# Kernel tuning notes

Measured on AMD Instinct MI355X. Metric: run time of the kernel, lower is better.

Reference implementation:

```python
import jax, jax.numpy as jnp
import numpy as np

HIDDEN_SIZE = 1024  # used for scaling, per the module's __init__
NEG_INF = -1e9

def setup_inputs() -> dict:
    key = jax.random.key(0)
    kq, kk, kv, km = jax.random.split(key, 4)
    B, H, S, D = 2, 16, 2048, 64
    query = jax.random.normal(kq, (B, H, S, D), dtype=jnp.float32)
    k_ = jax.random.normal(kk, (B, H, S, D), dtype=jnp.float32)
    v_ = jax.random.normal(kv, (B, H, S, D), dtype=jnp.float32)
    mask = jax.random.randint(km, (B, S), 0, 2, dtype=jnp.int32)
    return {"query": query, "key": k_, "value": v_, "mask": mask}

def reference(query, key, value, mask):
    # scores: [B,H,S,S]
    scores = jnp.einsum("bhqd,bhkd->bhqk", query, key)
    scores = scores / jnp.sqrt(jnp.float32(HIDDEN_SIZE))
    m = mask.astype(jnp.float32)[:, None, None, :]  # [B,1,1,S]
    scores = scores + NEG_INF * (1.0 - m)
    weights = jax.nn.softmax(scores, axis=-1)
    return jnp.einsum("bhqk,bhkd->bhqd", weights, value)
```

## Files before the change

kernel.cpp:

```cpp
#include <hip/hip_runtime.h>
#include <hip/hip_bf16.h>

typedef __bf16 bf16x8 __attribute__((ext_vector_type(8)));
typedef __bf16 bf16x4 __attribute__((ext_vector_type(4)));
typedef float  f32x4  __attribute__((ext_vector_type(4)));

constexpr int SEQ = 2048;
constexpr int HD  = 64;
constexpr int KT  = 64;
constexpr int QB  = 64;
constexpr int NT  = SEQ / KT;
constexpr int LDP = 72;

__global__ __launch_bounds__(256)
void prepass(const float* __restrict__ K, const float* __restrict__ V,
             __bf16* __restrict__ Kf, __bf16* __restrict__ Vf)
{
    const int t = blockIdx.x, bh = blockIdx.y, tid = threadIdx.x;
    const size_t base = (size_t)bh * SEQ * HD;
    __bf16* kd = Kf + (size_t)(bh * NT + t) * 4096;
    __bf16* vd = Vf + (size_t)(bh * NT + t) * 4096;

    #pragma unroll
    for (int p = 0; p < 2; ++p) {
        int gran = p * 256 + tid;
        int frag = gran >> 6, l = gran & 63, lo = l & 15, hi = l >> 4;
        int s = frag >> 1, kh = frag & 1;
        const float* src = K + base + (size_t)(t*64 + s*16 + lo) * HD + kh*32 + hi*8;
        float4 a = *(const float4*)src, c = *(const float4*)(src + 4);
        bf16x8 o;
        o[0]=(__bf16)a.x; o[1]=(__bf16)a.y; o[2]=(__bf16)a.z; o[3]=(__bf16)a.w;
        o[4]=(__bf16)c.x; o[5]=(__bf16)c.y; o[6]=(__bf16)c.z; o[7]=(__bf16)c.w;
        *(bf16x8*)(kd + gran * 8) = o;
    }
    #pragma unroll
    for (int p = 0; p < 2; ++p) {
        int gran = p * 256 + tid;
        int frag = gran >> 6, l = gran & 63, lo = l & 15, hi = l >> 4;
        int nt = frag >> 1, kh = frag & 1;
        const float* src = V + base + (size_t)(t*64 + kh*32 + hi*8) * HD + nt*16 + lo;
        bf16x8 o;
        #pragma unroll
        for (int j = 0; j < 8; ++j) o[j] = (__bf16)src[j * HD];
        *(bf16x8*)(vd + gran * 8) = o;
    }
}

__global__ __launch_bounds__(256, 4)
void attn_fwd3(const float* __restrict__ Q, const __bf16* __restrict__ Kf,
               const __bf16* __restrict__ Vf, const int* __restrict__ mask,
               float* __restrict__ out)
{
    __shared__ __bf16 Pl[4][16][LDP];
    __shared__ unsigned long long Ml[NT];

    const int tid = threadIdx.x;
    const int w   = tid >> 6;
    const int l   = tid & 63;
    const int lo  = l & 15;
    const int hi  = l >> 4;

    const int id   = blockIdx.x;
    const int virt = (id & 7) * 128 + (id >> 3);
    const int bh   = virt >> 5;
    const int qb   = virt & 31;
    const int b    = bh >> 4;
    const size_t base = (size_t)bh * SEQ * HD;
    const int qbase = qb * QB + w * 16;

    {
        const int4* mp = (const int4*)(mask + b * SEQ);
        int4 m0 = mp[tid * 2], m1 = mp[tid * 2 + 1];
        unsigned byte =
            ((unsigned)(m0.x != 0)     ) | ((unsigned)(m0.y != 0) << 1) |
            ((unsigned)(m0.z != 0) << 2) | ((unsigned)(m0.w != 0) << 3) |
            ((unsigned)(m1.x != 0) << 4) | ((unsigned)(m1.y != 0) << 5) |
            ((unsigned)(m1.z != 0) << 6) | ((unsigned)(m1.w != 0) << 7);
        ((unsigned char*)Ml)[tid] = (unsigned char)byte;
    }

    bf16x8 qf[2];
    {
        const float* qp = Q + base + (size_t)(qbase + lo) * HD;
        #pragma unroll
        for (int kh = 0; kh < 2; ++kh) {
            const float4 a = *(const float4*)(qp + kh*32 + hi*8);
            const float4 c = *(const float4*)(qp + kh*32 + hi*8 + 4);
            bf16x8 f;
            f[0]=(__bf16)a.x; f[1]=(__bf16)a.y; f[2]=(__bf16)a.z; f[3]=(__bf16)a.w;
            f[4]=(__bf16)c.x; f[5]=(__bf16)c.y; f[6]=(__bf16)c.z; f[7]=(__bf16)c.w;
            qf[kh] = f;
        }
    }

    __syncthreads();

    f32x4 acc[4] = {{0,0,0,0},{0,0,0,0},{0,0,0,0},{0,0,0,0}};
    float m_run = -INFINITY, l_run = 0.f;

    const __bf16* Kb = Kf + (size_t)bh * NT * 4096 + l * 8;
    const __bf16* Vb = Vf + (size_t)bh * NT * 4096 + l * 8;

    for (int t = 0; t < NT; ++t) {
        const __bf16* Kt = Kb + (size_t)t * 4096;
        const __bf16* Vt = Vb + (size_t)t * 4096;

        float sv[4][4];
        const unsigned long long mb = Ml[t];
        #pragma unroll
        for (int s = 0; s < 4; ++s) {
            bf16x8 k0 = *(const bf16x8*)(Kt + (s*2+0) * 512);
            bf16x8 k1 = *(const bf16x8*)(Kt + (s*2+1) * 512);
            f32x4 c = {0,0,0,0};
            c = __builtin_amdgcn_mfma_f32_16x16x32_bf16(k0, qf[0], c, 0, 0, 0);
            c = __builtin_amdgcn_mfma_f32_16x16x32_bf16(k1, qf[1], c, 0, 0, 0);
            const unsigned ms = (unsigned)(mb >> (s * 16));
            #pragma unroll
            for (int r = 0; r < 4; ++r)
                sv[s][r] = c[r] * 0.03125f +
                           (((ms >> (hi*4 + r)) & 1u) ? 0.f : -1e9f);
        }

        bf16x8 vfr[8];
        #pragma unroll
        for (int f = 0; f < 8; ++f) vfr[f] = *(const bf16x8*)(Vt + f * 512);

        float tmx[4], tsm[4];
        #pragma unroll
        for (int s = 0; s < 4; ++s)
            tmx[s] = fmaxf(fmaxf(sv[s][0], sv[s][1]), fmaxf(sv[s][2], sv[s][3]));
        float pm = fmaxf(fmaxf(tmx[0], tmx[1]), fmaxf(tmx[2], tmx[3]));
        pm = fmaxf(pm, __shfl_xor(pm, 16));
        pm = fmaxf(pm, __shfl_xor(pm, 32));

        const float mn  = fmaxf(m_run, pm);
        const float scl = __expf(m_run - mn);
        m_run = mn;

        float p[4][4];
        #pragma unroll
        for (int s = 0; s < 4; ++s) {
            #pragma unroll
            for (int r = 0; r < 4; ++r)
                p[s][r] = __expf(sv[s][r] - mn);
            tsm[s] = (p[s][0] + p[s][1]) + (p[s][2] + p[s][3]);
        }
        float rs = (tsm[0] + tsm[1]) + (tsm[2] + tsm[3]);
        rs += __shfl_xor(rs, 16);
        rs += __shfl_xor(rs, 32);
        l_run = l_run * scl + rs;

        #pragma unroll
        for (int nt = 0; nt < 4; ++nt)
            #pragma unroll
            for (int r = 0; r < 4; ++r)
                acc[nt][r] *= scl;

        #pragma unroll
        for (int s = 0; s < 4; ++s)
            #pragma unroll
            for (int r = 0; r < 4; ++r)
                Pl[w][lo][s*16 + hi*4 + r] = (__bf16)p[s][r];

        bf16x8 pa0 = *(const bf16x8*)&Pl[w][lo][hi * 8];
        bf16x8 pa1 = *(const bf16x8*)&Pl[w][lo][32 + hi * 8];
        #pragma unroll
        for (int nt = 0; nt < 4; ++nt) {
            acc[nt] = __builtin_amdgcn_mfma_f32_16x16x32_bf16(vfr[nt*2+0], pa0, acc[nt], 0, 0, 0);
            acc[nt] = __builtin_amdgcn_mfma_f32_16x16x32_bf16(vfr[nt*2+1], pa1, acc[nt], 0, 0, 0);
        }
    }

    const float inv = 1.0f / l_run;
    float* op = out + base + (size_t)(qbase + lo) * HD;
    #pragma unroll
    for (int nt = 0; nt < 4; ++nt)
        #pragma unroll
        for (int r = 0; r < 4; ++r)
            op[nt*16 + hi*4 + r] = acc[nt][r] * inv;
}

__global__ __launch_bounds__(256)
void attn_fwd_legacy(const float* __restrict__ Q, const float* __restrict__ K,
                     const float* __restrict__ V, const int* __restrict__ mask,
                     float* __restrict__ out)
{
    __shared__ __bf16 Kl[KT][LDP];
    __shared__ __bf16 Vl[HD][LDP];
    __shared__ __bf16 Pl[4][16][LDP];

    const int tid = threadIdx.x;
    const int w   = tid >> 6;
    const int l   = tid & 63;
    const int lo  = l & 15;
    const int hi  = l >> 4;

    const int bh = blockIdx.y;
    const int b  = bh >> 4;
    const size_t base = (size_t)bh * SEQ * HD;
    const int qbase = blockIdx.x * QB + w * 16;

    bf16x8 qf[2];
    {
        const float* qp = Q + base + (size_t)(qbase + lo) * HD;
        #pragma unroll
        for (int kh = 0; kh < 2; ++kh) {
            const float4 a = *(const float4*)(qp + kh*32 + hi*8);
            const float4 c = *(const float4*)(qp + kh*32 + hi*8 + 4);
            bf16x8 f;
            f[0]=(__bf16)a.x; f[1]=(__bf16)a.y; f[2]=(__bf16)a.z; f[3]=(__bf16)a.w;
            f[4]=(__bf16)c.x; f[5]=(__bf16)c.y; f[6]=(__bf16)c.z; f[7]=(__bf16)c.w;
            qf[kh] = f;
        }
    }

    f32x4 acc[4] = {{0,0,0,0},{0,0,0,0},{0,0,0,0},{0,0,0,0}};
    float m_run[4], l_run[4];
    #pragma unroll
    for (int r = 0; r < 4; ++r) { m_run[r] = -INFINITY; l_run[r] = 0.f; }

    const int* maskp = mask + b * SEQ;

    for (int k0 = 0; k0 < SEQ; k0 += KT) {
        #pragma unroll
        for (int i = 0; i < 4; ++i) {
            int e4 = i * 256 + tid;
            int key = e4 >> 4, d4 = (e4 & 15) * 4;
            float4 kv = *(const float4*)(K + base + (size_t)(k0 + key) * HD + d4);
            bf16x4 kb;
            kb[0]=(__bf16)kv.x; kb[1]=(__bf16)kv.y; kb[2]=(__bf16)kv.z; kb[3]=(__bf16)kv.w;
            *(bf16x4*)&Kl[key][d4] = kb;
        }
        #pragma unroll
        for (int i = 0; i < 4; ++i) {
            int e4 = i * 256 + tid;
            int key = e4 >> 4, d4 = (e4 & 15) * 4;
            float4 vv = *(const float4*)(V + base + (size_t)(k0 + key) * HD + d4);
            Vl[d4+0][key] = (__bf16)vv.x;
            Vl[d4+1][key] = (__bf16)vv.y;
            Vl[d4+2][key] = (__bf16)vv.z;
            Vl[d4+3][key] = (__bf16)vv.w;
        }
        __syncthreads();

        float sv[4][4];
        #pragma unroll
        for (int s = 0; s < 4; ++s) {
            f32x4 c = {0,0,0,0};
            bf16x8 kf0 = *(const bf16x8*)&Kl[s*16 + lo][hi*8];
            bf16x8 kf1 = *(const bf16x8*)&Kl[s*16 + lo][32 + hi*8];
            c = __builtin_amdgcn_mfma_f32_16x16x32_bf16(qf[0], kf0, c, 0, 0, 0);
            c = __builtin_amdgcn_mfma_f32_16x16x32_bf16(qf[1], kf1, c, 0, 0, 0);
            const int km = maskp[k0 + s*16 + lo];
            #pragma unroll
            for (int r = 0; r < 4; ++r)
                sv[s][r] = km ? (c[r] * 0.03125f) : -1e9f;
        }

        float tm[4];
        #pragma unroll
        for (int r = 0; r < 4; ++r)
            tm[r] = fmaxf(fmaxf(sv[0][r], sv[1][r]), fmaxf(sv[2][r], sv[3][r]));
        #pragma unroll
        for (int off = 1; off < 16; off <<= 1)
            #pragma unroll
            for (int r = 0; r < 4; ++r)
                tm[r] = fmaxf(tm[r], __shfl_xor(tm[r], off));

        float scl[4];
        #pragma unroll
        for (int r = 0; r < 4; ++r) {
            float mn = fmaxf(m_run[r], tm[r]);
            scl[r] = __expf(m_run[r] - mn);
            m_run[r] = mn;
        }
        float pv_[4][4], rs[4] = {0.f, 0.f, 0.f, 0.f};
        #pragma unroll
        for (int s = 0; s < 4; ++s)
            #pragma unroll
            for (int r = 0; r < 4; ++r) {
                float p = __expf(sv[s][r] - m_run[r]);
                pv_[s][r] = p;
                rs[r] += p;
            }
        #pragma unroll
        for (int off = 1; off < 16; off <<= 1)
            #pragma unroll
            for (int r = 0; r < 4; ++r)
                rs[r] += __shfl_xor(rs[r], off);
        #pragma unroll
        for (int r = 0; r < 4; ++r)
            l_run[r] = l_run[r] * scl[r] + rs[r];
        #pragma unroll
        for (int nt = 0; nt < 4; ++nt)
            #pragma unroll
            for (int r = 0; r < 4; ++r)
                acc[nt][r] *= scl[r];

        #pragma unroll
        for (int s = 0; s < 4; ++s)
            #pragma unroll
            for (int r = 0; r < 4; ++r)
                Pl[w][hi*4 + r][s*16 + lo] = (__bf16)pv_[s][r];

        bf16x8 pa0 = *(const bf16x8*)&Pl[w][lo][hi*8];
        bf16x8 pa1 = *(const bf16x8*)&Pl[w][lo][32 + hi*8];
        #pragma unroll
        for (int nt = 0; nt < 4; ++nt) {
            bf16x8 v0 = *(const bf16x8*)&Vl[nt*16 + lo][hi*8];
            bf16x8 v1 = *(const bf16x8*)&Vl[nt*16 + lo][32 + hi*8];
            acc[nt] = __builtin_amdgcn_mfma_f32_16x16x32_bf16(pa0, v0, acc[nt], 0, 0, 0);
            acc[nt] = __builtin_amdgcn_mfma_f32_16x16x32_bf16(pa1, v1, acc[nt], 0, 0, 0);
        }
        __syncthreads();
    }

    float inv[4];
    #pragma unroll
    for (int r = 0; r < 4; ++r) inv[r] = 1.0f / l_run[r];
    float* op = out + base + (size_t)qbase * HD;
    #pragma unroll
    for (int nt = 0; nt < 4; ++nt)
        #pragma unroll
        for (int r = 0; r < 4; ++r)
            op[(size_t)(hi*4 + r) * HD + nt*16 + lo] = acc[nt][r] * inv[r];
}

extern "C" void kernel_launch(void* const* d_in, const int* in_sizes, int n_in,
                              void* d_out, int out_size, void* d_ws, size_t ws_size,
                              hipStream_t stream) {
    (void)in_sizes; (void)n_in; (void)out_size;
    const float* Q  = (const float*)d_in[0];
    const float* K  = (const float*)d_in[1];
    const float* V  = (const float*)d_in[2];
    const int* mask = (const int*)d_in[3];
    float* out      = (float*)d_out;

    const size_t kv_elems = (size_t)32 * SEQ * HD;
    const size_t need = kv_elems * 2  * 2 ;

    if (ws_size >= need) {
        __bf16* Kf = (__bf16*)d_ws;
        __bf16* Vf = Kf + kv_elems;
        hipLaunchKernelGGL(prepass, dim3(NT, 32), dim3(256), 0, stream, K, V, Kf, Vf);
        hipLaunchKernelGGL(attn_fwd3, dim3(1024), dim3(256), 0, stream,
                           Q, Kf, Vf, mask, out);
    } else {
        hipLaunchKernelGGL(attn_fwd_legacy, dim3(SEQ / QB, 32), dim3(256), 0, stream,
                           Q, K, V, mask, out);
    }
}
```

Baseline: 168.7 us.

## Add lazy softmax rescaling, deferred row-sum reduction, setprio, and LDS-staged prepass

The online-softmax loop now skips the cross-lane max reduction and accumulator rescale unless some lane's tile max exceeds the running max by more than 8. The per-tile row-sum shuffles are replaced by per-lane partial sums that are reduced once at the end. The P matrix is written to LDS as packed bf16x4 stores, and s_setprio brackets the MFMA sections. The K/V prepass stages tiles through shared memory so the V transpose reads coalesced global data, at the cost of an extra LDS round trip and barrier.

After: 161.2 us. -4.5%, faster.

```diff
diff --git a/kernel.cpp b/kernel.cpp
--- a/kernel.cpp
+++ b/kernel.cpp
@@ -16,33 +16,41 @@
 void prepass(const float* __restrict__ K, const float* __restrict__ V,
              __bf16* __restrict__ Kf, __bf16* __restrict__ Vf)
 {
+    __shared__ __bf16 Kt[64][72];
+    __shared__ __bf16 Vt[64][72];
+
     const int t = blockIdx.x, bh = blockIdx.y, tid = threadIdx.x;
-    const size_t base = (size_t)bh * SEQ * HD;
+    const size_t base = (size_t)bh * SEQ * HD + (size_t)t * 64 * HD;
+
+    #pragma unroll
+    for (int p = 0; p < 4; ++p) {
+        int idx = p * 256 + tid;
+        int row = idx >> 4, c4 = (idx & 15) * 4;
+        float4 kv = *(const float4*)(K + base + row * HD + c4);
+        bf16x4 kb;
+        kb[0]=(__bf16)kv.x; kb[1]=(__bf16)kv.y; kb[2]=(__bf16)kv.z; kb[3]=(__bf16)kv.w;
+        *(bf16x4*)&Kt[row][c4] = kb;
+        float4 vv = *(const float4*)(V + base + row * HD + c4);
+        bf16x4 vb;
+        vb[0]=(__bf16)vv.x; vb[1]=(__bf16)vv.y; vb[2]=(__bf16)vv.z; vb[3]=(__bf16)vv.w;
+        *(bf16x4*)&Vt[row][c4] = vb;
+    }
+    __syncthreads();
+
     __bf16* kd = Kf + (size_t)(bh * NT + t) * 4096;
     __bf16* vd = Vf + (size_t)(bh * NT + t) * 4096;
-
     #pragma unroll
     for (int p = 0; p < 2; ++p) {
         int gran = p * 256 + tid;
         int frag = gran >> 6, l = gran & 63, lo = l & 15, hi = l >> 4;
         int s = frag >> 1, kh = frag & 1;
-        const float* src = K + base + (size_t)(t*64 + s*16 + lo) * HD + kh*32 + hi*8;
-        float4 a = *(const float4*)src, c = *(const float4*)(src + 4);
-        bf16x8 o;
-        o[0]=(__bf16)a.x; o[1]=(__bf16)a.y; o[2]=(__bf16)a.z; o[3]=(__bf16)a.w;
-        o[4]=(__bf16)c.x; o[5]=(__bf16)c.y; o[6]=(__bf16)c.z; o[7]=(__bf16)c.w;
-        *(bf16x8*)(kd + gran * 8) = o;
-    }
-    #pragma unroll
-    for (int p = 0; p < 2; ++p) {
-        int gran = p * 256 + tid;
-        int frag = gran >> 6, l = gran & 63, lo = l & 15, hi = l >> 4;
-        int nt = frag >> 1, kh = frag & 1;
-        const float* src = V + base + (size_t)(t*64 + kh*32 + hi*8) * HD + nt*16 + lo;
-        bf16x8 o;
-        #pragma unroll
-        for (int j = 0; j < 8; ++j) o[j] = (__bf16)src[j * HD];
-        *(bf16x8*)(vd + gran * 8) = o;
+        bf16x8 ko = *(const bf16x8*)&Kt[s*16 + lo][kh*32 + hi*8];
+        *(bf16x8*)(kd + gran * 8) = ko;
+        bf16x8 vo;
+        #pragma unroll
+        for (int j = 0; j < 8; ++j)
+            vo[j] = Vt[kh*32 + hi*8 + j][s*16 + lo];
+        *(bf16x8*)(vd + gran * 8) = vo;
     }
 }
 
@@ -96,7 +104,8 @@
     __syncthreads();
 
     f32x4 acc[4] = {{0,0,0,0},{0,0,0,0},{0,0,0,0},{0,0,0,0}};
-    float m_run = -INFINITY, l_run = 0.f;
+    float m_run  = -INFINITY;
+    float l_part = 0.f;
 
     const __bf16* Kb = Kf + (size_t)bh * NT * 4096 + l * 8;
     const __bf16* Vb = Vf + (size_t)bh * NT * 4096 + l * 8;
@@ -107,6 +116,7 @@
 
         float sv[4][4];
         const unsigned long long mb = Ml[t];
+        __builtin_amdgcn_s_setprio(1);
         #pragma unroll
         for (int s = 0; s < 4; ++s) {
             bf16x8 k0 = *(const bf16x8*)(Kt + (s*2+0) * 512);
@@ -120,58 +130,69 @@
                 sv[s][r] = c[r] * 0.03125f +
                            (((ms >> (hi*4 + r)) & 1u) ? 0.f : -1e9f);
         }
+        __builtin_amdgcn_s_setprio(0);
 
         bf16x8 vfr[8];
         #pragma unroll
         for (int f = 0; f < 8; ++f) vfr[f] = *(const bf16x8*)(Vt + f * 512);
 
-        float tmx[4], tsm[4];
+        float pm = sv[0][0];
         #pragma unroll
         for (int s = 0; s < 4; ++s)
-            tmx[s] = fmaxf(fmaxf(sv[s][0], sv[s][1]), fmaxf(sv[s][2], sv[s][3]));
-        float pm = fmaxf(fmaxf(tmx[0], tmx[1]), fmaxf(tmx[2], tmx[3]));
-        pm = fmaxf(pm, __shfl_xor(pm, 16));
-        pm = fmaxf(pm, __shfl_xor(pm, 32));
-
-        const float mn  = fmaxf(m_run, pm);
-        const float scl = __expf(m_run - mn);
-        m_run = mn;
-
-        float p[4][4];
+            #pragma unroll
+            for (int r = 0; r < 4; ++r)
+                pm = fmaxf(pm, sv[s][r]);
+
+        if (!__all(pm - m_run <= 8.0f)) {
+            float pmr = pm;
+            pmr = fmaxf(pmr, __shfl_xor(pmr, 16));
+            pmr = fmaxf(pmr, __shfl_xor(pmr, 32));
+            const float mn  = fmaxf(m_run, pmr);
+            const float scl = __expf(m_run - mn);
+            m_run = mn;
+            l_part *= scl;
+            #pragma unroll
+            for (int nt = 0; nt < 4; ++nt)
+                #pragma unroll
+                for (int r = 0; r < 4; ++r)
+                    acc[nt][r] *= scl;
+        }
+
+        float p[4][4], ls = 0.f;
         #pragma unroll
         for (int s = 0; s < 4; ++s) {
             #pragma unroll
-            for (int r = 0; r < 4; ++r)
-                p[s][r] = __expf(sv[s][r] - mn);
-            tsm[s] = (p[s][0] + p[s][1]) + (p[s][2] + p[s][3]);
-        }
-        float rs = (tsm[0] + tsm[1]) + (tsm[2] + tsm[3]);
-        rs += __shfl_xor(rs, 16);
-        rs += __shfl_xor(rs, 32);
-        l_run = l_run * scl + rs;
-
-        #pragma unroll
-        for (int nt = 0; nt < 4; ++nt)
-            #pragma unroll
-            for (int r = 0; r < 4; ++r)
-                acc[nt][r] *= scl;
-
-        #pragma unroll
-        for (int s = 0; s < 4; ++s)
-            #pragma unroll
-            for (int r = 0; r < 4; ++r)
-                Pl[w][lo][s*16 + hi*4 + r] = (__bf16)p[s][r];
+            for (int r = 0; r < 4; ++r) {
+                p[s][r] = __expf(sv[s][r] - m_run);
+                ls += p[s][r];
+            }
+        }
+        l_part += ls;
+
+        #pragma unroll
+        for (int s = 0; s < 4; ++s) {
+            bf16x4 pk;
+            pk[0]=(__bf16)p[s][0]; pk[1]=(__bf16)p[s][1];
+            pk[2]=(__bf16)p[s][2]; pk[3]=(__bf16)p[s][3];
+            *(bf16x4*)&Pl[w][lo][s*16 + hi*4] = pk;
+        }
 
         bf16x8 pa0 = *(const bf16x8*)&Pl[w][lo][hi * 8];
         bf16x8 pa1 = *(const bf16x8*)&Pl[w][lo][32 + hi * 8];
+        __builtin_amdgcn_s_setprio(1);
         #pragma unroll
         for (int nt = 0; nt < 4; ++nt) {
             acc[nt] = __builtin_amdgcn_mfma_f32_16x16x32_bf16(vfr[nt*2+0], pa0, acc[nt], 0, 0, 0);
             acc[nt] = __builtin_amdgcn_mfma_f32_16x16x32_bf16(vfr[nt*2+1], pa1, acc[nt], 0, 0, 0);
         }
-    }
-
-    const float inv = 1.0f / l_run;
+        __builtin_amdgcn_s_setprio(0);
+    }
+
+    float lr = l_part;
+    lr += __shfl_xor(lr, 16);
+    lr += __shfl_xor(lr, 32);
+    const float inv = 1.0f / lr;
+
     float* op = out + base + (size_t)(qbase + lo) * HD;
     #pragma unroll
     for (int nt = 0; nt < 4; ++nt)
```
